# Performance work log

Measured on AMD Instinct MI355X. Metric: run time of the kernel, lower is better.

Reference implementation:

```python
import jax, jax.numpy as jnp
import numpy as np

HEAD_DIM = 256
HIDDEN = 1536
INTERMEDIATE = 6144
NUM_KV_HEADS = 1
NUM_Q_HEADS = 8
SCALE = HEAD_DIM ** (-0.5)
PAST_LEN = 8191


def setup_inputs() -> dict:
    key = jax.random.key(0)
    ks = jax.random.split(key, 20)
    def lin(ki, fan_in, fan_out):
        # torch nn.Linear init: U(-1/sqrt(fan_in), 1/sqrt(fan_in)); stored (in, out) for x @ W
        bound = 1.0 / np.sqrt(fan_in)
        W = jax.random.uniform(ki, (fan_in, fan_out), jnp.float32, -bound, bound)
        b = jax.random.uniform(jax.random.fold_in(ki, 1), (fan_out,), jnp.float32, -bound, bound)
        return W, b
    Wq, bq = lin(ks[0], HIDDEN, NUM_Q_HEADS * HEAD_DIM)
    Wk, bk = lin(ks[1], HIDDEN, NUM_KV_HEADS * HEAD_DIM)
    Wv, bv = lin(ks[2], HIDDEN, NUM_KV_HEADS * HEAD_DIM)
    Wo, bo = lin(ks[3], NUM_Q_HEADS * HEAD_DIM, HIDDEN)
    Wg, bg = lin(ks[4], HIDDEN, INTERMEDIATE)
    Wu, bu = lin(ks[5], HIDDEN, INTERMEDIATE)
    Wd, bd = lin(ks[6], INTERMEDIATE, HIDDEN)
    x = jax.random.normal(ks[7], (1, 1, HIDDEN), jnp.float32)
    k_past = jax.random.normal(ks[8], (1, NUM_KV_HEADS, PAST_LEN, HEAD_DIM), jnp.float32)
    v_past = jax.random.normal(ks[9], (1, NUM_KV_HEADS, PAST_LEN, HEAD_DIM), jnp.float32)
    return dict(x=x, k_past=k_past, v_past=v_past,
                Wq=Wq, bq=bq, Wk=Wk, bk=bk, Wv=Wv, bv=bv, Wo=Wo, bo=bo,
                Wg=Wg, bg=bg, Wu=Wu, bu=bu, Wd=Wd, bd=bd)


def reference(x, k_past, v_past, Wq, bq, Wk, bk, Wv, bv, Wo, bo, Wg, bg, Wu, bu, Wd, bd):
    residual = x
    # projections; q: (1, Hq, 1, D), k/v: (1, Hkv, 1, D)
    q = (x @ Wq + bq).reshape(1, 1, NUM_Q_HEADS, HEAD_DIM).transpose(0, 2, 1, 3)
    k = (x @ Wk + bk).reshape(1, 1, NUM_KV_HEADS, HEAD_DIM).transpose(0, 2, 1, 3)
    v = (x @ Wv + bv).reshape(1, 1, NUM_KV_HEADS, HEAD_DIM).transpose(0, 2, 1, 3)
    k_full = jnp.concatenate([k_past, k], axis=2)  # (1, Hkv, S, D)
    v_full = jnp.concatenate([v_past, v], axis=2)
    # GQA: broadcast the single KV head across 8 Q heads (no materialized repeat)
    scores = jnp.einsum('bhqd,bksd->bhqs', q, k_full) * SCALE  # (1, Hq, 1, S)
    attn = jax.nn.softmax(scores, axis=-1)
    out = jnp.einsum('bhqs,bksd->bhqd', attn, v_full)  # (1, Hq, 1, D)
    out = out.transpose(0, 2, 1, 3).reshape(1, 1, NUM_Q_HEADS * HEAD_DIM)
    out = out @ Wo + bo
    x = residual + out
    # MLP: GELU(gate) * up -> down (exact erf GELU, matching torch nn.GELU default)
    ffn = (jax.nn.gelu(x @ Wg + bg, approximate=False) * (x @ Wu + bu)) @ Wd + bd
    return x + ffn
```

## Files before the change

kernel.cpp:

```cpp
#include <hip/hip_runtime.h>
#include <hip/hip_bf16.h>
#include <math.h>

#define PAST 8191
#define SCALEF 0.0625f

using bf = __hip_bfloat16;

__device__ __forceinline__ float bf2f(unsigned short u) {
    return __uint_as_float(((unsigned)u) << 16);
}
__device__ __forceinline__ void unpack8(uint4 r, float* f) {
    f[0] = __uint_as_float(r.x << 16);
    f[1] = __uint_as_float(r.x & 0xffff0000u);
    f[2] = __uint_as_float(r.y << 16);
    f[3] = __uint_as_float(r.y & 0xffff0000u);
    f[4] = __uint_as_float(r.z << 16);
    f[5] = __uint_as_float(r.z & 0xffff0000u);
    f[6] = __uint_as_float(r.w << 16);
    f[7] = __uint_as_float(r.w & 0xffff0000u);
}

template<bool BF16>
__device__ __forceinline__ void load8(const void* W, size_t off, float* f) {
    if constexpr (BF16) {
        uint4 r = *reinterpret_cast<const uint4*>((const unsigned short*)W + off);
        unpack8(r, f);
    } else {
        const float* p = (const float*)W + off;
        float4 a = *reinterpret_cast<const float4*>(p);
        float4 b = *reinterpret_cast<const float4*>(p + 4);
        f[0]=a.x; f[1]=a.y; f[2]=a.z; f[3]=a.w;
        f[4]=b.x; f[5]=b.y; f[6]=b.z; f[7]=b.w;
    }
}
template<bool BF16>
__device__ __forceinline__ void load4(const void* P, size_t off, float* f) {
    if constexpr (BF16) {
        uint2 r = *reinterpret_cast<const uint2*>((const unsigned short*)P + off);
        f[0] = __uint_as_float(r.x << 16); f[1] = __uint_as_float(r.x & 0xffff0000u);
        f[2] = __uint_as_float(r.y << 16); f[3] = __uint_as_float(r.y & 0xffff0000u);
    } else {
        float4 a = *reinterpret_cast<const float4*>((const float*)P + off);
        f[0]=a.x; f[1]=a.y; f[2]=a.z; f[3]=a.w;
    }
}
template<bool BF16>
__device__ __forceinline__ float load1(const void* P, int i) {
    if constexpr (BF16) return bf2f(((const unsigned short*)P)[i]);
    else return ((const float*)P)[i];
}

__global__ __launch_bounds__(256) void probe_kernel(const unsigned int* __restrict__ xw,
                                                    int* __restrict__ flag) {
    __shared__ int cnt;
    if (threadIdx.x == 0) cnt = 0;
    __syncthreads();
    int ok = 0;
    for (int i = threadIdx.x; i < 768; i += 256) {
        unsigned e = (xw[i] >> 7) & 0xff;
        if (e >= 96 && e <= 142) ok++;
    }
    atomicAdd(&cnt, ok);
    __syncthreads();
    if (threadIdx.x == 0) *flag = (cnt > 500) ? 1 : 0;
}

template<bool BF16>
__device__ __forceinline__ void gemv_rows32(const void* __restrict__ W, int ldw,
                                            const float* __restrict__ xs_wave,
                                            int row0, int j, float acc[8]) {
    #pragma unroll
    for (int i = 0; i < 32; i += 8) {
        float f[8][8];
        #pragma unroll
        for (int r = 0; r < 8; ++r)
            load8<BF16>(W, (size_t)(row0 + i + r) * ldw + j, f[r]);
        #pragma unroll
        for (int r = 0; r < 8; ++r) {
            float xv = xs_wave[i + r];
            #pragma unroll
            for (int q = 0; q < 8; ++q) acc[q] = fmaf(xv, f[r][q], acc[q]);
        }
    }
}

__device__ __forceinline__ void block_reduce_512(float acc[8], float* red,
                                                 int wave, int lane) {
    if (wave > 0) {
        float* dst = red + (wave - 1) * 512 + lane * 8;
        #pragma unroll
        for (int q = 0; q < 8; ++q) dst[q] = acc[q];
    }
    __syncthreads();
    if (wave == 0) {
        int o = lane * 8;
        #pragma unroll
        for (int q = 0; q < 8; ++q)
            acc[q] += red[o + q] + red[512 + o + q] + red[1024 + o + q];
    }
}

template<bool BF16>
__device__ void qkv_body(const void* __restrict__ x, const void* __restrict__ Wq,
                         const void* __restrict__ bq, const void* __restrict__ Wk,
                         const void* __restrict__ bk, const void* __restrict__ Wv,
                         const void* __restrict__ bv, float* __restrict__ qkv) {
    __shared__ float xs[128];
    __shared__ float red[3 * 512];
    int tid = threadIdx.x, wave = tid >> 6, lane = tid & 63;
    int i0 = blockIdx.y * 128;
    if (tid < 128) xs[tid] = load1<BF16>(x, i0 + tid);
    __syncthreads();
    int j = blockIdx.x * 512 + lane * 8;
    const void* W; const void* bias; int ldw, jl;
    if (j < 2048)      { W = Wq; bias = bq; ldw = 2048; jl = j; }
    else if (j < 2304) { W = Wk; bias = bk; ldw = 256;  jl = j - 2048; }
    else               { W = Wv; bias = bv; ldw = 256;  jl = j - 2304; }
    float acc[8] = {0,0,0,0,0,0,0,0};
    gemv_rows32<BF16>(W, ldw, xs + wave * 32, i0 + wave * 32, jl, acc);
    block_reduce_512(acc, red, wave, lane);
    if (wave == 0) {
        if (blockIdx.y == 0) {
            #pragma unroll
            for (int q = 0; q < 8; ++q) acc[q] += load1<BF16>(bias, jl + q);
        }
        #pragma unroll
        for (int q = 0; q < 8; ++q) atomicAdd(&qkv[j + q], acc[q]);
    }
}
__global__ __launch_bounds__(256) void qkv_kernel(
    const void* x, const void* Wq, const void* bq, const void* Wk, const void* bk,
    const void* Wv, const void* bv, float* qkv, const int* flag) {
    if (*flag) qkv_body<true>(x, Wq, bq, Wk, bk, Wv, bv, qkv);
    else       qkv_body<false>(x, Wq, bq, Wk, bk, Wv, bv, qkv);
}

template<bool BF16>
__device__ void scores_body(const float* __restrict__ qkv, const void* __restrict__ k_past,
                            float* __restrict__ s) {
    int wave = threadIdx.x >> 6, lane = threadIdx.x & 63;
    int p = blockIdx.x * 4 + wave;
    int d0 = lane * 4;
    float kf[4];
    if (p < PAST) {
        load4<BF16>(k_past, (size_t)p * 256 + d0, kf);
    } else {
        kf[0] = qkv[2048 + d0];     kf[1] = qkv[2048 + d0 + 1];
        kf[2] = qkv[2048 + d0 + 2]; kf[3] = qkv[2048 + d0 + 3];
    }
    float part[8];
    #pragma unroll
    for (int h = 0; h < 8; ++h) {
        const float* qh = qkv + h * 256 + d0;
        part[h] = qh[0]*kf[0] + qh[1]*kf[1] + qh[2]*kf[2] + qh[3]*kf[3];
    }
    #pragma unroll
    for (int m = 1; m < 64; m <<= 1) {
        #pragma unroll
        for (int h = 0; h < 8; ++h) part[h] += __shfl_xor(part[h], m, 64);
    }
    if (lane == 0) {
        #pragma unroll
        for (int h = 0; h < 8; ++h) s[h * 8192 + p] = part[h] * SCALEF;
    }
}
__global__ __launch_bounds__(256) void scores_kernel(
    const float* qkv, const void* k_past, float* s, const int* flag) {
    if (*flag) scores_body<true>(qkv, k_past, s);
    else       scores_body<false>(qkv, k_past, s);
}

__global__ __launch_bounds__(256) void mred_kernel(
    const float* __restrict__ s, float* __restrict__ ml) {
    __shared__ float red[256];
    int h = blockIdx.x, tid = threadIdx.x;
    const float* sh = s + h * 8192;
    float m = -1e30f;
    for (int p = tid; p < 8192; p += 256) m = fmaxf(m, sh[p]);
    red[tid] = m; __syncthreads();
    for (int w = 128; w > 0; w >>= 1) {
        if (tid < w) red[tid] = fmaxf(red[tid], red[tid + w]);
        __syncthreads();
    }
    m = red[0]; __syncthreads();
    float l = 0.f;
    for (int p = tid; p < 8192; p += 256) l += expf(sh[p] - m);
    red[tid] = l; __syncthreads();
    for (int w = 128; w > 0; w >>= 1) {
        if (tid < w) red[tid] += red[tid + w];
        __syncthreads();
    }
    if (tid == 0) { ml[2 * h] = m; ml[2 * h + 1] = red[0]; }
}

template<bool BF16>
__device__ void pv_body(const float* __restrict__ s, const float* __restrict__ ml,
                        const void* __restrict__ v_past, const float* __restrict__ qkv,
                        float* __restrict__ attnout) {
    __shared__ float ss[1024];
    __shared__ float red[3 * 2048];
    int tid = threadIdx.x, wave = tid >> 6, lane = tid & 63;
    int base = blockIdx.x * 128;
    #pragma unroll
    for (int idx = tid; idx < 1024; idx += 256) {
        int h = idx >> 7, t = idx & 127;
        ss[idx] = expf(s[h * 8192 + base + t] - ml[2 * h]);
    }
    __syncthreads();
    int d0 = lane * 4;
    float o[8][4];
    #pragma unroll
    for (int h = 0; h < 8; ++h)
        #pragma unroll
        for (int r = 0; r < 4; ++r) o[h][r] = 0.f;
    int p0 = base + wave * 32;
    for (int it = 0; it < 32; it += 4) {
        float vf[4][4];
        if (p0 + it + 3 < PAST) {
            #pragma unroll
            for (int r = 0; r < 4; ++r)
                load4<BF16>(v_past, (size_t)(p0 + it + r) * 256 + d0, vf[r]);
        } else {
            #pragma unroll
            for (int r = 0; r < 4; ++r) {
                int p = p0 + it + r;
                if (p < PAST) {
                    load4<BF16>(v_past, (size_t)p * 256 + d0, vf[r]);
                } else {
                    vf[r][0] = qkv[2304 + d0];     vf[r][1] = qkv[2304 + d0 + 1];
                    vf[r][2] = qkv[2304 + d0 + 2]; vf[r][3] = qkv[2304 + d0 + 3];
                }
            }
        }
        #pragma unroll
        for (int r = 0; r < 4; ++r) {
            int t = wave * 32 + it + r;
            #pragma unroll
            for (int h = 0; h < 8; ++h) {
                float w = ss[h * 128 + t];
                #pragma unroll
                for (int rr = 0; rr < 4; ++rr) o[h][rr] = fmaf(w, vf[r][rr], o[h][rr]);
            }
        }
    }
    if (wave > 0) {
        float* dst = red + (wave - 1) * 2048;
        #pragma unroll
        for (int h = 0; h < 8; ++h)
            #pragma unroll
            for (int r = 0; r < 4; ++r) dst[h * 256 + d0 + r] = o[h][r];
    }
    __syncthreads();
    if (wave == 0) {
        #pragma unroll
        for (int h = 0; h < 8; ++h)
            #pragma unroll
            for (int r = 0; r < 4; ++r) {
                float v = o[h][r] + red[h*256 + d0 + r] + red[2048 + h*256 + d0 + r]
                        + red[4096 + h*256 + d0 + r];
                atomicAdd(&attnout[h * 256 + d0 + r], v);
            }
    }
}
__global__ __launch_bounds__(256) void pv_kernel(
    const float* s, const float* ml, const void* v_past, const float* qkv,
    float* attnout, const int* flag) {
    if (*flag) pv_body<true>(s, ml, v_past, qkv, attnout);
    else       pv_body<false>(s, ml, v_past, qkv, attnout);
}

template<bool BF16>
__device__ void oproj_body(const float* __restrict__ attnout, const float* __restrict__ ml,
                           const void* __restrict__ Wo, const void* __restrict__ bo,
                           const void* __restrict__ xin, float* __restrict__ x2) {
    __shared__ float xs[128];
    __shared__ float red[3 * 512];
    int tid = threadIdx.x, wave = tid >> 6, lane = tid & 63;
    int i0 = blockIdx.y * 128;
    if (tid < 128) {
        int i = i0 + tid;
        xs[tid] = attnout[i] * (1.0f / ml[2 * (i >> 8) + 1]);
    }
    __syncthreads();
    int j = blockIdx.x * 512 + lane * 8;
    float acc[8] = {0,0,0,0,0,0,0,0};
    gemv_rows32<BF16>(Wo, 1536, xs + wave * 32, i0 + wave * 32, j, acc);
    block_reduce_512(acc, red, wave, lane);
    if (wave == 0) {
        if (blockIdx.y == 0) {
            #pragma unroll
            for (int q = 0; q < 8; ++q)
                acc[q] += load1<BF16>(bo, j + q) + load1<BF16>(xin, j + q);
        }
        #pragma unroll
        for (int q = 0; q < 8; ++q) atomicAdd(&x2[j + q], acc[q]);
    }
}
__global__ __launch_bounds__(256) void oproj_kernel(
    const float* attnout, const float* ml, const void* Wo, const void* bo,
    const void* xin, float* x2, const int* flag) {
    if (*flag) oproj_body<true>(attnout, ml, Wo, bo, xin, x2);
    else       oproj_body<false>(attnout, ml, Wo, bo, xin, x2);
}

template<bool BF16>
__device__ void gateup_body(const float* __restrict__ x2, const void* __restrict__ Wg,
                            const void* __restrict__ Wu, float* __restrict__ gacc,
                            float* __restrict__ uacc) {
    __shared__ float xs[128];
    __shared__ float red[3 * 512];
    int tid = threadIdx.x, wave = tid >> 6, lane = tid & 63;
    int i0 = blockIdx.y * 128;
    if (tid < 128) xs[tid] = x2[i0 + tid];
    __syncthreads();
    const void* W = blockIdx.z ? Wu : Wg;
    float* out = blockIdx.z ? uacc : gacc;
    int j = blockIdx.x * 512 + lane * 8;
    float acc[8] = {0,0,0,0,0,0,0,0};
    gemv_rows32<BF16>(W, 6144, xs + wave * 32, i0 + wave * 32, j, acc);
    block_reduce_512(acc, red, wave, lane);
    if (wave == 0) {
        #pragma unroll
        for (int q = 0; q < 8; ++q) atomicAdd(&out[j + q], acc[q]);
    }
}
__global__ __launch_bounds__(256) void gateup_kernel(
    const float* x2, const void* Wg, const void* Wu, float* gacc, float* uacc,
    const int* flag) {
    if (*flag) gateup_body<true>(x2, Wg, Wu, gacc, uacc);
    else       gateup_body<false>(x2, Wg, Wu, gacc, uacc);
}

template<bool BF16>
__device__ void down_body(const float* __restrict__ gacc, const float* __restrict__ uacc,
                          const void* __restrict__ bg, const void* __restrict__ bu,
                          const void* __restrict__ Wd, float* __restrict__ yacc) {
    __shared__ float xs[128];
    __shared__ float red[3 * 512];
    int tid = threadIdx.x, wave = tid >> 6, lane = tid & 63;
    int i0 = blockIdx.y * 128;
    if (tid < 128) {
        int i = i0 + tid;
        float g = gacc[i] + load1<BF16>(bg, i);
        float u = uacc[i] + load1<BF16>(bu, i);
        float ge = 0.5f * g * (1.0f + erff(g * 0.70710678118654752f));
        xs[tid] = ge * u;
    }
    __syncthreads();
    int j = blockIdx.x * 512 + lane * 8;
    float acc[8] = {0,0,0,0,0,0,0,0};
    gemv_rows32<BF16>(Wd, 1536, xs + wave * 32, i0 + wave * 32, j, acc);
    block_reduce_512(acc, red, wave, lane);
    if (wave == 0) {
        #pragma unroll
        for (int q = 0; q < 8; ++q) atomicAdd(&yacc[j + q], acc[q]);
    }
}
__global__ __launch_bounds__(256) void down_kernel(
    const float* gacc, const float* uacc, const void* bg, const void* bu,
    const void* Wd, float* yacc, const int* flag) {
    if (*flag) down_body<true>(gacc, uacc, bg, bu, Wd, yacc);
    else       down_body<false>(gacc, uacc, bg, bu, Wd, yacc);
}

__global__ __launch_bounds__(256) void final_kernel(
    const float* __restrict__ x2, const float* __restrict__ yacc,
    const void* __restrict__ bd, void* __restrict__ out, const int* __restrict__ flag) {
    int j = blockIdx.x * 256 + threadIdx.x;
    if (j < 1536) {
        int isbf = *flag;
        float b = isbf ? bf2f(((const unsigned short*)bd)[j]) : ((const float*)bd)[j];
        float v = x2[j] + yacc[j] + b;
        if (isbf) ((bf*)out)[j] = __float2bfloat16(v);
        else      ((float*)out)[j] = v;
    }
}

extern "C" void kernel_launch(void* const* d_in, const int* in_sizes, int n_in,
                              void* d_out, int out_size, void* d_ws, size_t ws_size,
                              hipStream_t stream) {
    const void* x  = d_in[0];
    const void* kp = d_in[1];
    const void* vp = d_in[2];
    const void* Wq = d_in[3];
    const void* bq = d_in[4];
    const void* Wk = d_in[5];
    const void* bk = d_in[6];
    const void* Wv = d_in[7];
    const void* bv = d_in[8];
    const void* Wo = d_in[9];
    const void* bo = d_in[10];
    const void* Wg = d_in[11];
    const void* bg = d_in[12];
    const void* Wu = d_in[13];
    const void* bu = d_in[14];
    const void* Wd = d_in[15];
    const void* bd = d_in[16];

    float* ws      = (float*)d_ws;
    float* qkv     = ws;
    float* x2      = ws + 2560;
    float* gacc    = ws + 4096;
    float* uacc    = ws + 10240;
    float* yacc    = ws + 16384;
    float* attnout = ws + 17920;
    float* ml      = ws + 19968;
    float* sc      = ws + 20480;
    int*  flag     = (int*)(ws + 86016);

    hipMemsetAsync(ws, 0, 19968 * sizeof(float), stream);
    probe_kernel<<<1, 256, 0, stream>>>((const unsigned int*)x, flag);

    qkv_kernel<<<dim3(5, 12), 256, 0, stream>>>(x, Wq, bq, Wk, bk, Wv, bv, qkv, flag);
    scores_kernel<<<2048, 256, 0, stream>>>(qkv, kp, sc, flag);
    mred_kernel<<<8, 256, 0, stream>>>(sc, ml);
    pv_kernel<<<64, 256, 0, stream>>>(sc, ml, vp, qkv, attnout, flag);
    oproj_kernel<<<dim3(3, 16), 256, 0, stream>>>(attnout, ml, Wo, bo, x, x2, flag);
    gateup_kernel<<<dim3(12, 12, 2), 256, 0, stream>>>(x2, Wg, Wu, gacc, uacc, flag);
    down_kernel<<<dim3(3, 48), 256, 0, stream>>>(gacc, uacc, bg, bu, Wd, yacc, flag);
    final_kernel<<<6, 256, 0, stream>>>(x2, yacc, bd, d_out, flag);
}
```

Before: 278.8 us.

## Drop softmax max pass, fuse exp into scores, split GEMVs across more blocks

```diff
diff --git a/kernel.cpp b/kernel.cpp
--- a/kernel.cpp
+++ b/kernel.cpp
@@ -52,36 +52,39 @@
 }
 
 __global__ __launch_bounds__(256) void probe_kernel(const unsigned int* __restrict__ xw,
+                                                    float* __restrict__ zws,
                                                     int* __restrict__ flag) {
-    __shared__ int cnt;
-    if (threadIdx.x == 0) cnt = 0;
-    __syncthreads();
-    int ok = 0;
-    for (int i = threadIdx.x; i < 768; i += 256) {
-        unsigned e = (xw[i] >> 7) & 0xff;
-        if (e >= 96 && e <= 142) ok++;
-    }
-    atomicAdd(&cnt, ok);
-    __syncthreads();
-    if (threadIdx.x == 0) *flag = (cnt > 500) ? 1 : 0;
-}
-
-template<bool BF16>
-__device__ __forceinline__ void gemv_rows32(const void* __restrict__ W, int ldw,
-                                            const float* __restrict__ xs_wave,
-                                            int row0, int j, float acc[8]) {
-    #pragma unroll
-    for (int i = 0; i < 32; i += 8) {
-        float f[8][8];
-        #pragma unroll
-        for (int r = 0; r < 8; ++r)
-            load8<BF16>(W, (size_t)(row0 + i + r) * ldw + j, f[r]);
-        #pragma unroll
-        for (int r = 0; r < 8; ++r) {
-            float xv = xs_wave[i + r];
-            #pragma unroll
-            for (int q = 0; q < 8; ++q) acc[q] = fmaf(xv, f[r][q], acc[q]);
-        }
+    int idx = blockIdx.x * 256 + threadIdx.x;
+    #pragma unroll
+    for (int k = idx; k < 20480; k += 10240) zws[k] = 0.f;
+    if (blockIdx.x == 0) {
+        __shared__ int cnt;
+        if (threadIdx.x == 0) cnt = 0;
+        __syncthreads();
+        int ok = 0;
+        for (int i = threadIdx.x; i < 768; i += 256) {
+            unsigned e = (xw[i] >> 7) & 0xff;
+            if (e >= 96 && e <= 142) ok++;
+        }
+        atomicAdd(&cnt, ok);
+        __syncthreads();
+        if (threadIdx.x == 0) *flag = (cnt > 500) ? 1 : 0;
+    }
+}
+
+template<bool BF16>
+__device__ __forceinline__ void gemv_rows8(const void* __restrict__ W, int ldw,
+                                           const float* __restrict__ xs_wave,
+                                           int row0, int j, float acc[8]) {
+    float f[8][8];
+    #pragma unroll
+    for (int r = 0; r < 8; ++r)
+        load8<BF16>(W, (size_t)(row0 + r) * ldw + j, f[r]);
+    #pragma unroll
+    for (int r = 0; r < 8; ++r) {
+        float xv = xs_wave[r];
+        #pragma unroll
+        for (int q = 0; q < 8; ++q) acc[q] = fmaf(xv, f[r][q], acc[q]);
     }
 }
 
@@ -106,11 +109,11 @@
                          const void* __restrict__ bq, const void* __restrict__ Wk,
                          const void* __restrict__ bk, const void* __restrict__ Wv,
                          const void* __restrict__ bv, float* __restrict__ qkv) {
-    __shared__ float xs[128];
+    __shared__ float xs[32];
     __shared__ float red[3 * 512];
     int tid = threadIdx.x, wave = tid >> 6, lane = tid & 63;
-    int i0 = blockIdx.y * 128;
-    if (tid < 128) xs[tid] = load1<BF16>(x, i0 + tid);
+    int i0 = blockIdx.y * 32;
+    if (tid < 32) xs[tid] = load1<BF16>(x, i0 + tid);
     __syncthreads();
     int j = blockIdx.x * 512 + lane * 8;
     const void* W; const void* bias; int ldw, jl;
@@ -118,7 +121,7 @@
     else if (j < 2304) { W = Wk; bias = bk; ldw = 256;  jl = j - 2048; }
     else               { W = Wv; bias = bv; ldw = 256;  jl = j - 2304; }
     float acc[8] = {0,0,0,0,0,0,0,0};
-    gemv_rows32<BF16>(W, ldw, xs + wave * 32, i0 + wave * 32, jl, acc);
+    gemv_rows8<BF16>(W, ldw, xs + wave * 8, i0 + wave * 8, jl, acc);
     block_reduce_512(acc, red, wave, lane);
     if (wave == 0) {
         if (blockIdx.y == 0) {
@@ -138,8 +141,11 @@
 
 template<bool BF16>
 __device__ void scores_body(const float* __restrict__ qkv, const void* __restrict__ k_past,
-                            float* __restrict__ s) {
-    int wave = threadIdx.x >> 6, lane = threadIdx.x & 63;
+                            float* __restrict__ s, float* __restrict__ lpart) {
+    __shared__ float wsum[8];
+    int tid = threadIdx.x, wave = tid >> 6, lane = tid & 63;
+    if (tid < 8) wsum[tid] = 0.f;
+    __syncthreads();
     int p = blockIdx.x * 4 + wave;
     int d0 = lane * 4;
     float kf[4];
@@ -162,50 +168,32 @@
     }
     if (lane == 0) {
         #pragma unroll
-        for (int h = 0; h < 8; ++h) s[h * 8192 + p] = part[h] * SCALEF;
-    }
+        for (int h = 0; h < 8; ++h) {
+            float w = expf(part[h] * SCALEF);
+            s[h * 8192 + p] = w;
+            atomicAdd(&wsum[h], w);
+        }
+    }
+    __syncthreads();
+    if (tid < 8) atomicAdd(&lpart[tid * 64 + (blockIdx.x & 63)], wsum[tid]);
 }
 __global__ __launch_bounds__(256) void scores_kernel(
-    const float* qkv, const void* k_past, float* s, const int* flag) {
-    if (*flag) scores_body<true>(qkv, k_past, s);
-    else       scores_body<false>(qkv, k_past, s);
-}
-
-__global__ __launch_bounds__(256) void mred_kernel(
-    const float* __restrict__ s, float* __restrict__ ml) {
-    __shared__ float red[256];
-    int h = blockIdx.x, tid = threadIdx.x;
-    const float* sh = s + h * 8192;
-    float m = -1e30f;
-    for (int p = tid; p < 8192; p += 256) m = fmaxf(m, sh[p]);
-    red[tid] = m; __syncthreads();
-    for (int w = 128; w > 0; w >>= 1) {
-        if (tid < w) red[tid] = fmaxf(red[tid], red[tid + w]);
-        __syncthreads();
-    }
-    m = red[0]; __syncthreads();
-    float l = 0.f;
-    for (int p = tid; p < 8192; p += 256) l += expf(sh[p] - m);
-    red[tid] = l; __syncthreads();
-    for (int w = 128; w > 0; w >>= 1) {
-        if (tid < w) red[tid] += red[tid + w];
-        __syncthreads();
-    }
-    if (tid == 0) { ml[2 * h] = m; ml[2 * h + 1] = red[0]; }
-}
-
-template<bool BF16>
-__device__ void pv_body(const float* __restrict__ s, const float* __restrict__ ml,
-                        const void* __restrict__ v_past, const float* __restrict__ qkv,
-                        float* __restrict__ attnout) {
-    __shared__ float ss[1024];
+    const float* qkv, const void* k_past, float* s, float* lpart, const int* flag) {
+    if (*flag) scores_body<true>(qkv, k_past, s, lpart);
+    else       scores_body<false>(qkv, k_past, s, lpart);
+}
+
+template<bool BF16>
+__device__ void pv_body(const float* __restrict__ s, const void* __restrict__ v_past,
+                        const float* __restrict__ qkv, float* __restrict__ attnout) {
+    __shared__ float ss[512];
     __shared__ float red[3 * 2048];
     int tid = threadIdx.x, wave = tid >> 6, lane = tid & 63;
-    int base = blockIdx.x * 128;
-    #pragma unroll
-    for (int idx = tid; idx < 1024; idx += 256) {
-        int h = idx >> 7, t = idx & 127;
-        ss[idx] = expf(s[h * 8192 + base + t] - ml[2 * h]);
+    int base = blockIdx.x * 64;
+    #pragma unroll
+    for (int idx = tid; idx < 512; idx += 256) {
+        int h = idx >> 6, t = idx & 63;
+        ss[idx] = s[h * 8192 + base + t];
     }
     __syncthreads();
     int d0 = lane * 4;
@@ -214,8 +202,8 @@
     for (int h = 0; h < 8; ++h)
         #pragma unroll
         for (int r = 0; r < 4; ++r) o[h][r] = 0.f;
-    int p0 = base + wave * 32;
-    for (int it = 0; it < 32; it += 4) {
+    int p0 = base + wave * 16;
+    for (int it = 0; it < 16; it += 4) {
         float vf[4][4];
         if (p0 + it + 3 < PAST) {
             #pragma unroll
@@ -235,10 +223,10 @@
         }
         #pragma unroll
         for (int r = 0; r < 4; ++r) {
-            int t = wave * 32 + it + r;
+            int t = wave * 16 + it + r;
             #pragma unroll
             for (int h = 0; h < 8; ++h) {
-                float w = ss[h * 128 + t];
+                float w = ss[h * 64 + t];
                 #pragma unroll
                 for (int rr = 0; rr < 4; ++rr) o[h][rr] = fmaf(w, vf[r][rr], o[h][rr]);
             }
@@ -264,28 +252,31 @@
     }
 }
 __global__ __launch_bounds__(256) void pv_kernel(
-    const float* s, const float* ml, const void* v_past, const float* qkv,
-    float* attnout, const int* flag) {
-    if (*flag) pv_body<true>(s, ml, v_past, qkv, attnout);
-    else       pv_body<false>(s, ml, v_past, qkv, attnout);
-}
-
-template<bool BF16>
-__device__ void oproj_body(const float* __restrict__ attnout, const float* __restrict__ ml,
+    const float* s, const void* v_past, const float* qkv, float* attnout,
+    const int* flag) {
+    if (*flag) pv_body<true>(s, v_past, qkv, attnout);
+    else       pv_body<false>(s, v_past, qkv, attnout);
+}
+
+template<bool BF16>
+__device__ void oproj_body(const float* __restrict__ attnout, const float* __restrict__ lpart,
                            const void* __restrict__ Wo, const void* __restrict__ bo,
                            const void* __restrict__ xin, float* __restrict__ x2) {
-    __shared__ float xs[128];
+    __shared__ float xs[32];
     __shared__ float red[3 * 512];
     int tid = threadIdx.x, wave = tid >> 6, lane = tid & 63;
-    int i0 = blockIdx.y * 128;
-    if (tid < 128) {
-        int i = i0 + tid;
-        xs[tid] = attnout[i] * (1.0f / ml[2 * (i >> 8) + 1]);
+    int i0 = blockIdx.y * 32;
+    int h = i0 >> 8;
+    if (tid < 64) {
+        float v = lpart[h * 64 + tid];
+        #pragma unroll
+        for (int m = 1; m < 64; m <<= 1) v += __shfl_xor(v, m, 64);
+        if (tid < 32) xs[tid] = attnout[i0 + tid] * (1.0f / v);
     }
     __syncthreads();
     int j = blockIdx.x * 512 + lane * 8;
     float acc[8] = {0,0,0,0,0,0,0,0};
-    gemv_rows32<BF16>(Wo, 1536, xs + wave * 32, i0 + wave * 32, j, acc);
+    gemv_rows8<BF16>(Wo, 1536, xs + wave * 8, i0 + wave * 8, j, acc);
     block_reduce_512(acc, red, wave, lane);
     if (wave == 0) {
         if (blockIdx.y == 0) {
@@ -298,27 +289,27 @@
     }
 }
 __global__ __launch_bounds__(256) void oproj_kernel(
-    const float* attnout, const float* ml, const void* Wo, const void* bo,
+    const float* attnout, const float* lpart, const void* Wo, const void* bo,
     const void* xin, float* x2, const int* flag) {
-    if (*flag) oproj_body<true>(attnout, ml, Wo, bo, xin, x2);
-    else       oproj_body<false>(attnout, ml, Wo, bo, xin, x2);
+    if (*flag) oproj_body<true>(attnout, lpart, Wo, bo, xin, x2);
+    else       oproj_body<false>(attnout, lpart, Wo, bo, xin, x2);
 }
 
 template<bool BF16>
 __device__ void gateup_body(const float* __restrict__ x2, const void* __restrict__ Wg,
                             const void* __restrict__ Wu, float* __restrict__ gacc,
                             float* __restrict__ uacc) {
-    __shared__ float xs[128];
+    __shared__ float xs[32];
     __shared__ float red[3 * 512];
     int tid = threadIdx.x, wave = tid >> 6, lane = tid & 63;
-    int i0 = blockIdx.y * 128;
-    if (tid < 128) xs[tid] = x2[i0 + tid];
+    int i0 = blockIdx.y * 32;
+    if (tid < 32) xs[tid] = x2[i0 + tid];
     __syncthreads();
     const void* W = blockIdx.z ? Wu : Wg;
     float* out = blockIdx.z ? uacc : gacc;
     int j = blockIdx.x * 512 + lane * 8;
     float acc[8] = {0,0,0,0,0,0,0,0};
-    gemv_rows32<BF16>(W, 6144, xs + wave * 32, i0 + wave * 32, j, acc);
+    gemv_rows8<BF16>(W, 6144, xs + wave * 8, i0 + wave * 8, j, acc);
     block_reduce_512(acc, red, wave, lane);
     if (wave == 0) {
         #pragma unroll
@@ -336,11 +327,11 @@
 __device__ void down_body(const float* __restrict__ gacc, const float* __restrict__ uacc,
                           const void* __restrict__ bg, const void* __restrict__ bu,
                           const void* __restrict__ Wd, float* __restrict__ yacc) {
-    __shared__ float xs[128];
+    __shared__ float xs[32];
     __shared__ float red[3 * 512];
     int tid = threadIdx.x, wave = tid >> 6, lane = tid & 63;
-    int i0 = blockIdx.y * 128;
-    if (tid < 128) {
+    int i0 = blockIdx.y * 32;
+    if (tid < 32) {
         int i = i0 + tid;
         float g = gacc[i] + load1<BF16>(bg, i);
         float u = uacc[i] + load1<BF16>(bu, i);
@@ -350,7 +341,7 @@
     __syncthreads();
     int j = blockIdx.x * 512 + lane * 8;
     float acc[8] = {0,0,0,0,0,0,0,0};
-    gemv_rows32<BF16>(Wd, 1536, xs + wave * 32, i0 + wave * 32, j, acc);
+    gemv_rows8<BF16>(Wd, 1536, xs + wave * 8, i0 + wave * 8, j, acc);
     block_reduce_512(acc, red, wave, lane);
     if (wave == 0) {
         #pragma unroll
@@ -405,19 +396,17 @@
     float* uacc    = ws + 10240;
     float* yacc    = ws + 16384;
     float* attnout = ws + 17920;
-    float* ml      = ws + 19968;
+    float* lpart   = ws + 19968;
     float* sc      = ws + 20480;
     int*  flag     = (int*)(ws + 86016);
 
-    hipMemsetAsync(ws, 0, 19968 * sizeof(float), stream);
-    probe_kernel<<<1, 256, 0, stream>>>((const unsigned int*)x, flag);
-
-    qkv_kernel<<<dim3(5, 12), 256, 0, stream>>>(x, Wq, bq, Wk, bk, Wv, bv, qkv, flag);
-    scores_kernel<<<2048, 256, 0, stream>>>(qkv, kp, sc, flag);
-    mred_kernel<<<8, 256, 0, stream>>>(sc, ml);
-    pv_kernel<<<64, 256, 0, stream>>>(sc, ml, vp, qkv, attnout, flag);
-    oproj_kernel<<<dim3(3, 16), 256, 0, stream>>>(attnout, ml, Wo, bo, x, x2, flag);
-    gateup_kernel<<<dim3(12, 12, 2), 256, 0, stream>>>(x2, Wg, Wu, gacc, uacc, flag);
-    down_kernel<<<dim3(3, 48), 256, 0, stream>>>(gacc, uacc, bg, bu, Wd, yacc, flag);
+    probe_kernel<<<40, 256, 0, stream>>>((const unsigned int*)x, ws, flag);
+
+    qkv_kernel<<<dim3(5, 48), 256, 0, stream>>>(x, Wq, bq, Wk, bk, Wv, bv, qkv, flag);
+    scores_kernel<<<2048, 256, 0, stream>>>(qkv, kp, sc, lpart, flag);
+    pv_kernel<<<128, 256, 0, stream>>>(sc, vp, qkv, attnout, flag);
+    oproj_kernel<<<dim3(3, 64), 256, 0, stream>>>(attnout, lpart, Wo, bo, x, x2, flag);
+    gateup_kernel<<<dim3(12, 48, 2), 256, 0, stream>>>(x2, Wg, Wu, gacc, uacc, flag);
+    down_kernel<<<dim3(3, 192), 256, 0, stream>>>(gacc, uacc, bg, bu, Wd, yacc, flag);
     final_kernel<<<6, 256, 0, stream>>>(x2, yacc, bd, d_out, flag);
 }
```

Result: slower. 312.7 us (+12.1%).

## Fuse scores, softmax reduction and PV into one attention kernel without max

Applied to the files above, without the earlier changes.

```diff
diff --git a/kernel.cpp b/kernel.cpp
--- a/kernel.cpp
+++ b/kernel.cpp
@@ -52,18 +52,24 @@
 }
 
 __global__ __launch_bounds__(256) void probe_kernel(const unsigned int* __restrict__ xw,
+                                                    float* __restrict__ zws,
                                                     int* __restrict__ flag) {
-    __shared__ int cnt;
-    if (threadIdx.x == 0) cnt = 0;
-    __syncthreads();
-    int ok = 0;
-    for (int i = threadIdx.x; i < 768; i += 256) {
-        unsigned e = (xw[i] >> 7) & 0xff;
-        if (e >= 96 && e <= 142) ok++;
-    }
-    atomicAdd(&cnt, ok);
-    __syncthreads();
-    if (threadIdx.x == 0) *flag = (cnt > 500) ? 1 : 0;
+    int idx = blockIdx.x * 256 + threadIdx.x;
+    #pragma unroll
+    for (int k = idx; k < 20480; k += 10240) zws[k] = 0.f;
+    if (blockIdx.x == 0) {
+        __shared__ int cnt;
+        if (threadIdx.x == 0) cnt = 0;
+        __syncthreads();
+        int ok = 0;
+        for (int i = threadIdx.x; i < 768; i += 256) {
+            unsigned e = (xw[i] >> 7) & 0xff;
+            if (e >= 96 && e <= 142) ok++;
+        }
+        atomicAdd(&cnt, ok);
+        __syncthreads();
+        if (threadIdx.x == 0) *flag = (cnt > 500) ? 1 : 0;
+    }
 }
 
 template<bool BF16>
@@ -137,112 +143,77 @@
 }
 
 template<bool BF16>
-__device__ void scores_body(const float* __restrict__ qkv, const void* __restrict__ k_past,
-                            float* __restrict__ s) {
-    int wave = threadIdx.x >> 6, lane = threadIdx.x & 63;
-    int p = blockIdx.x * 4 + wave;
+__device__ void attn_body(const float* __restrict__ qkv, const void* __restrict__ k_past,
+                          const void* __restrict__ v_past, float* __restrict__ attnout,
+                          float* __restrict__ lpart) {
+    __shared__ float wsum[8];
+    __shared__ float red[3 * 2048];
+    int tid = threadIdx.x, wave = tid >> 6, lane = tid & 63;
+    if (tid < 8) wsum[tid] = 0.f;
     int d0 = lane * 4;
-    float kf[4];
-    if (p < PAST) {
-        load4<BF16>(k_past, (size_t)p * 256 + d0, kf);
-    } else {
-        kf[0] = qkv[2048 + d0];     kf[1] = qkv[2048 + d0 + 1];
-        kf[2] = qkv[2048 + d0 + 2]; kf[3] = qkv[2048 + d0 + 3];
-    }
-    float part[8];
+    float4 qreg[8];
     #pragma unroll
-    for (int h = 0; h < 8; ++h) {
-        const float* qh = qkv + h * 256 + d0;
-        part[h] = qh[0]*kf[0] + qh[1]*kf[1] + qh[2]*kf[2] + qh[3]*kf[3];
-    }
-    #pragma unroll
-    for (int m = 1; m < 64; m <<= 1) {
-        #pragma unroll
-        for (int h = 0; h < 8; ++h) part[h] += __shfl_xor(part[h], m, 64);
-    }
-    if (lane == 0) {
-        #pragma unroll
-        for (int h = 0; h < 8; ++h) s[h * 8192 + p] = part[h] * SCALEF;
-    }
-}
-__global__ __launch_bounds__(256) void scores_kernel(
-    const float* qkv, const void* k_past, float* s, const int* flag) {
-    if (*flag) scores_body<true>(qkv, k_past, s);
-    else       scores_body<false>(qkv, k_past, s);
-}
-
-__global__ __launch_bounds__(256) void mred_kernel(
-    const float* __restrict__ s, float* __restrict__ ml) {
-    __shared__ float red[256];
-    int h = blockIdx.x, tid = threadIdx.x;
-    const float* sh = s + h * 8192;
-    float m = -1e30f;
-    for (int p = tid; p < 8192; p += 256) m = fmaxf(m, sh[p]);
-    red[tid] = m; __syncthreads();
-    for (int w = 128; w > 0; w >>= 1) {
-        if (tid < w) red[tid] = fmaxf(red[tid], red[tid + w]);
-        __syncthreads();
-    }
-    m = red[0]; __syncthreads();
-    float l = 0.f;
-    for (int p = tid; p < 8192; p += 256) l += expf(sh[p] - m);
-    red[tid] = l; __syncthreads();
-    for (int w = 128; w > 0; w >>= 1) {
-        if (tid < w) red[tid] += red[tid + w];
-        __syncthreads();
-    }
-    if (tid == 0) { ml[2 * h] = m; ml[2 * h + 1] = red[0]; }
-}
-
-template<bool BF16>
-__device__ void pv_body(const float* __restrict__ s, const float* __restrict__ ml,
-                        const void* __restrict__ v_past, const float* __restrict__ qkv,
-                        float* __restrict__ attnout) {
-    __shared__ float ss[1024];
-    __shared__ float red[3 * 2048];
-    int tid = threadIdx.x, wave = tid >> 6, lane = tid & 63;
-    int base = blockIdx.x * 128;
-    #pragma unroll
-    for (int idx = tid; idx < 1024; idx += 256) {
-        int h = idx >> 7, t = idx & 127;
-        ss[idx] = expf(s[h * 8192 + base + t] - ml[2 * h]);
-    }
-    __syncthreads();
-    int d0 = lane * 4;
+    for (int h = 0; h < 8; ++h)
+        qreg[h] = *reinterpret_cast<const float4*>(qkv + h * 256 + d0);
+    float4 knew = *reinterpret_cast<const float4*>(qkv + 2048 + d0);
+    float4 vnew = *reinterpret_cast<const float4*>(qkv + 2304 + d0);
+    __syncthreads();
+
     float o[8][4];
     #pragma unroll
     for (int h = 0; h < 8; ++h)
         #pragma unroll
         for (int r = 0; r < 4; ++r) o[h][r] = 0.f;
-    int p0 = base + wave * 32;
-    for (int it = 0; it < 32; it += 4) {
-        float vf[4][4];
-        if (p0 + it + 3 < PAST) {
-            #pragma unroll
-            for (int r = 0; r < 4; ++r)
+    float wl[8] = {0,0,0,0,0,0,0,0};
+
+    int p0 = blockIdx.x * 64 + wave * 16;
+    for (int it = 0; it < 16; it += 8) {
+        float kf[8][4], vf[8][4];
+        if (p0 + it + 7 < PAST) {
+            #pragma unroll
+            for (int r = 0; r < 8; ++r)
+                load4<BF16>(k_past, (size_t)(p0 + it + r) * 256 + d0, kf[r]);
+            #pragma unroll
+            for (int r = 0; r < 8; ++r)
                 load4<BF16>(v_past, (size_t)(p0 + it + r) * 256 + d0, vf[r]);
         } else {
             #pragma unroll
-            for (int r = 0; r < 4; ++r) {
+            for (int r = 0; r < 8; ++r) {
                 int p = p0 + it + r;
                 if (p < PAST) {
+                    load4<BF16>(k_past, (size_t)p * 256 + d0, kf[r]);
                     load4<BF16>(v_past, (size_t)p * 256 + d0, vf[r]);
                 } else {
-                    vf[r][0] = qkv[2304 + d0];     vf[r][1] = qkv[2304 + d0 + 1];
-                    vf[r][2] = qkv[2304 + d0 + 2]; vf[r][3] = qkv[2304 + d0 + 3];
+                    kf[r][0]=knew.x; kf[r][1]=knew.y; kf[r][2]=knew.z; kf[r][3]=knew.w;
+                    vf[r][0]=vnew.x; vf[r][1]=vnew.y; vf[r][2]=vnew.z; vf[r][3]=vnew.w;
                 }
             }
         }
         #pragma unroll
-        for (int r = 0; r < 4; ++r) {
-            int t = wave * 32 + it + r;
+        for (int r = 0; r < 8; ++r) {
+            float part[8];
             #pragma unroll
             for (int h = 0; h < 8; ++h) {
-                float w = ss[h * 128 + t];
+                part[h] = qreg[h].x*kf[r][0] + qreg[h].y*kf[r][1]
+                        + qreg[h].z*kf[r][2] + qreg[h].w*kf[r][3];
+            }
+            #pragma unroll
+            for (int m = 1; m < 64; m <<= 1) {
+                #pragma unroll
+                for (int h = 0; h < 8; ++h) part[h] += __shfl_xor(part[h], m, 64);
+            }
+            #pragma unroll
+            for (int h = 0; h < 8; ++h) {
+                float w = expf(part[h] * SCALEF);
+                wl[h] += w;
                 #pragma unroll
                 for (int rr = 0; rr < 4; ++rr) o[h][rr] = fmaf(w, vf[r][rr], o[h][rr]);
             }
         }
+    }
+    if (lane == 0) {
+        #pragma unroll
+        for (int h = 0; h < 8; ++h) atomicAdd(&wsum[h], wl[h]);
     }
     if (wave > 0) {
         float* dst = red + (wave - 1) * 2048;
@@ -262,25 +233,29 @@
                 atomicAdd(&attnout[h * 256 + d0 + r], v);
             }
     }
-}
-__global__ __launch_bounds__(256) void pv_kernel(
-    const float* s, const float* ml, const void* v_past, const float* qkv,
-    float* attnout, const int* flag) {
-    if (*flag) pv_body<true>(s, ml, v_past, qkv, attnout);
-    else       pv_body<false>(s, ml, v_past, qkv, attnout);
-}
-
-template<bool BF16>
-__device__ void oproj_body(const float* __restrict__ attnout, const float* __restrict__ ml,
+    if (tid < 8) atomicAdd(&lpart[tid * 64 + (blockIdx.x & 63)], wsum[tid]);
+}
+__global__ __launch_bounds__(256) void attn_kernel(
+    const float* qkv, const void* k_past, const void* v_past, float* attnout,
+    float* lpart, const int* flag) {
+    if (*flag) attn_body<true>(qkv, k_past, v_past, attnout, lpart);
+    else       attn_body<false>(qkv, k_past, v_past, attnout, lpart);
+}
+
+template<bool BF16>
+__device__ void oproj_body(const float* __restrict__ attnout, const float* __restrict__ lpart,
                            const void* __restrict__ Wo, const void* __restrict__ bo,
                            const void* __restrict__ xin, float* __restrict__ x2) {
     __shared__ float xs[128];
     __shared__ float red[3 * 512];
     int tid = threadIdx.x, wave = tid >> 6, lane = tid & 63;
     int i0 = blockIdx.y * 128;
+    int h = i0 >> 8;
     if (tid < 128) {
-        int i = i0 + tid;
-        xs[tid] = attnout[i] * (1.0f / ml[2 * (i >> 8) + 1]);
+        float v = lpart[h * 64 + (tid & 63)];
+        #pragma unroll
+        for (int m = 1; m < 64; m <<= 1) v += __shfl_xor(v, m, 64);
+        xs[tid] = attnout[i0 + tid] * (1.0f / v);
     }
     __syncthreads();
     int j = blockIdx.x * 512 + lane * 8;
@@ -298,10 +273,10 @@
     }
 }
 __global__ __launch_bounds__(256) void oproj_kernel(
-    const float* attnout, const float* ml, const void* Wo, const void* bo,
+    const float* attnout, const float* lpart, const void* Wo, const void* bo,
     const void* xin, float* x2, const int* flag) {
-    if (*flag) oproj_body<true>(attnout, ml, Wo, bo, xin, x2);
-    else       oproj_body<false>(attnout, ml, Wo, bo, xin, x2);
+    if (*flag) oproj_body<true>(attnout, lpart, Wo, bo, xin, x2);
+    else       oproj_body<false>(attnout, lpart, Wo, bo, xin, x2);
 }
 
 template<bool BF16>
@@ -405,18 +380,14 @@
     float* uacc    = ws + 10240;
     float* yacc    = ws + 16384;
     float* attnout = ws + 17920;
-    float* ml      = ws + 19968;
-    float* sc      = ws + 20480;
+    float* lpart   = ws + 19968;
     int*  flag     = (int*)(ws + 86016);
 
-    hipMemsetAsync(ws, 0, 19968 * sizeof(float), stream);
-    probe_kernel<<<1, 256, 0, stream>>>((const unsigned int*)x, flag);
+    probe_kernel<<<40, 256, 0, stream>>>((const unsigned int*)x, ws, flag);
 
     qkv_kernel<<<dim3(5, 12), 256, 0, stream>>>(x, Wq, bq, Wk, bk, Wv, bv, qkv, flag);
-    scores_kernel<<<2048, 256, 0, stream>>>(qkv, kp, sc, flag);
-    mred_kernel<<<8, 256, 0, stream>>>(sc, ml);
-    pv_kernel<<<64, 256, 0, stream>>>(sc, ml, vp, qkv, attnout, flag);
-    oproj_kernel<<<dim3(3, 16), 256, 0, stream>>>(attnout, ml, Wo, bo, x, x2, flag);
+    attn_kernel<<<128, 256, 0, stream>>>(qkv, kp, vp, attnout, lpart, flag);
+    oproj_kernel<<<dim3(3, 16), 256, 0, stream>>>(attnout, lpart, Wo, bo, x, x2, flag);
     gateup_kernel<<<dim3(12, 12, 2), 256, 0, stream>>>(x2, Wg, Wu, gacc, uacc, flag);
     down_kernel<<<dim3(3, 48), 256, 0, stream>>>(gacc, uacc, bg, bu, Wd, yacc, flag);
     final_kernel<<<6, 256, 0, stream>>>(x2, yacc, bd, d_out, flag);
```

Result: faster. 270.1 us (-3.1%).
